# Kernel optimization log

Measured on AMD Instinct MI355X. Metric: run time of the kernel, lower is better.

The kernel has to match this reference:

```python
import jax, jax.numpy as jnp
import numpy as np

E_QUBITS = 8  # embedding dim == number of qubits


def _iqp_amplitudes(x):
    """Statevector amplitudes of qml.IQPEmbedding(x) applied to |0..0>.

    x: [..., E] real. Returns [..., 2^E] complex64.
    Circuit: H on all wires, RZ(x_i) on wire i, MultiRZ(x_i*x_j) on all pairs i<j.
    For basis state z with signs s_i = (-1)^{z_i}:
      amp(z) = 2^{-E/2} * exp(i * phi(z)),
      phi(z) = -1/2 * sum_i x_i s_i - 1/2 * sum_{i<j} x_i x_j s_i s_j
             = -L/2 - (L^2 - ||x||^2)/4,  with L = sum_i x_i s_i.
    """
    E = x.shape[-1]
    z = jnp.arange(2 ** E)
    bits = (z[:, None] >> jnp.arange(E)[None, :]) & 1          # [2^E, E]
    s = (1.0 - 2.0 * bits).astype(x.dtype)                      # (-1)^{z_i}
    L = x @ s.T                                                 # [..., 2^E]
    sq = jnp.sum(x * x, axis=-1, keepdims=True)                 # ||x||^2
    phase = -0.5 * L - 0.25 * (L * L - sq)
    return jnp.exp(1j * phase) * (2.0 ** (-E / 2.0))            # complex64


def setup_inputs() -> dict:
    key = jax.random.key(0)
    kq, kk, kv = jax.random.split(key, 3)
    B, S, E = 16, 1024, E_QUBITS
    return {
        "Q": jax.random.normal(kq, (B, S, E), dtype=jnp.float32),
        "K": jax.random.normal(kk, (B, S, E), dtype=jnp.float32),
        "V": jax.random.normal(kv, (B, S, E), dtype=jnp.float32),
    }


def reference(Q, K, V):
    # Pure-state amplitudes for every token (IQP embedding). [B,S,2^E] complex
    aq = _iqp_amplitudes(Q)
    ak = _iqp_amplitudes(K)
    # Fidelity of pure states: |<psi_q|psi_k>|^2, batched Gram matrix.
    ip = jnp.einsum("bid,bjd->bij", jnp.conj(aq), ak)          # [B,S,S] complex
    fid = jnp.real(ip * jnp.conj(ip))                           # [B,S,S] float32
    attn = 2.0 * fid - 1.0
    return jnp.einsum("bij,bje->bie", attn, V)                  # [B,S,E]
```

## Files before the change

### kernel.cpp

```cpp
#include <hip/hip_runtime.h>
#include <hip/hip_bf16.h>
#include <stdint.h>

#define NB 16
#define S_LEN 1024
#define E_Q 8

typedef float v4f __attribute__((ext_vector_type(4)));
typedef short v8s __attribute__((ext_vector_type(8)));
typedef int   v4i __attribute__((ext_vector_type(4)));

__global__ __launch_bounds__(256) void build_tables(
    const float* __restrict__ Q, const float* __restrict__ K,
    int8_t* __restrict__ Aq, int8_t* __restrict__ Kt,
    float* __restrict__ out)
{
    const int which = blockIdx.y;
    const float* X = which ? K : Q;

    if (which == 0 && blockIdx.x < 128) {
        float4 z; z.x = z.y = z.z = z.w = 0.f;
        ((float4*)out)[blockIdx.x * 256 + threadIdx.x] = z;
    }

    const int tok = blockIdx.x * 16 + (threadIdx.x >> 4);
    const int hi  = threadIdx.x & 15;
    const int zb  = hi * 16;

    const float* x = X + tok * E_Q;
    float xv[E_Q]; float sq = 0.f;
#pragma unroll
    for (int i = 0; i < E_Q; ++i) { xv[i] = x[i]; sq += xv[i] * xv[i]; }
    const float qsq = 0.25f * sq;

    float L = xv[0] + xv[1] + xv[2] + xv[3];
#pragma unroll
    for (int i = 4; i < 8; ++i) L += ((hi >> (i - 4)) & 1) ? -xv[i] : xv[i];

    __align__(16) int8_t cb[16];
    __align__(16) int8_t sb[16];

    {
        const float phi = fmaf(-0.25f, L * L, fmaf(-0.5f, L, qsq));
        float s, c; __sincosf(phi, &s, &c);
        cb[0] = (int8_t)__float2int_rn(127.f * c);
        sb[0] = (int8_t)__float2int_rn(127.f * s);
    }
#pragma unroll
    for (int n = 1; n < 16; ++n) {
        const int g  = n ^ (n >> 1);
        const int gp = (n - 1) ^ ((n - 1) >> 1);
        const int t  = __builtin_ctz(g ^ gp);
        const float twox = 2.0f * xv[t];
        L = ((g >> t) & 1) ? (L - twox) : (L + twox);
        const float phi = fmaf(-0.25f, L * L, fmaf(-0.5f, L, qsq));
        float s, c; __sincosf(phi, &s, &c);
        cb[g] = (int8_t)__float2int_rn(127.f * c);
        sb[g] = (int8_t)__float2int_rn(127.f * s);
    }

    if (which == 0) {
        int8_t* dst = Aq + (size_t)tok * 512;
        *(uint4*)(dst + zb)       = *(const uint4*)cb;
        *(uint4*)(dst + 256 + zb) = *(const uint4*)sb;
    } else {
        __align__(16) int8_t nb[16];
#pragma unroll
        for (int i = 0; i < 16; ++i) nb[i] = (int8_t)(-cb[i]);
        int8_t* dst = Kt + (size_t)tok * 768;
        *(uint4*)(dst + zb)       = *(const uint4*)cb;
        *(uint4*)(dst + 256 + zb) = *(const uint4*)sb;
        *(uint4*)(dst + 512 + zb) = *(const uint4*)nb;
    }
}

__global__ __launch_bounds__(256, 2) void qk_pv(
    const int8_t* __restrict__ Aq, const int8_t* __restrict__ Kt,
    const float* __restrict__ V, float* __restrict__ out)
{
    __shared__ __align__(16) char smem[49152];
    int8_t* lA  = (int8_t*)smem;
    int8_t* lK0 = (int8_t*)(smem + 16384);
    int8_t* lK1 = (int8_t*)(smem + 32768);
    uint16_t* lattn = (uint16_t*)smem;
    uint16_t* lVt   = (uint16_t*)(smem + 34816);

    const int jblk = blockIdx.x, iblk = blockIdx.y, b = blockIdx.z;
    const int tid  = threadIdx.x;
    const int lane = tid & 63, wv = tid >> 6;
    const int wKj = wv >> 1, wQi = wv & 1;
    const int r15 = lane & 15, qq = lane >> 4;

    const int qsw   = (tid & 7) ^ ((tid >> 3) & 7);
    const int baseA = (tid >> 3) * 512 + qsw * 16;
    const int baseK = (tid >> 3) * 768 + qsw * 16;
    const int lbase = wv * 1024;

    const int8_t* gA = Aq + (size_t)(b * S_LEN + iblk * 128) * 512;
    const int8_t* gK = Kt + (size_t)(b * S_LEN + jblk * 128) * 768;

    v4i accRe[4][4], accIm[4][4];
#pragma unroll
    for (int nj = 0; nj < 4; ++nj)
#pragma unroll
        for (int mi = 0; mi < 4; ++mi) {
            accRe[nj][mi] = (v4i)0;
            accIm[nj][mi] = (v4i)0;
        }

    for (int c = 0; c < 4; ++c) {
        __syncthreads();
        const int cbyte = c * 128;
#pragma unroll
        for (int p = 0; p < 4; ++p) {
            const int lo = p * 4096 + lbase;
            __builtin_amdgcn_global_load_lds(
                (const __attribute__((address_space(1))) void*)(gA + cbyte + baseA + p * 16384),
                (__attribute__((address_space(3))) void*)(lA + lo), 16, 0, 0);
            __builtin_amdgcn_global_load_lds(
                (const __attribute__((address_space(1))) void*)(gK + cbyte + baseK + p * 24576),
                (__attribute__((address_space(3))) void*)(lK0 + lo), 16, 0, 0);
            __builtin_amdgcn_global_load_lds(
                (const __attribute__((address_space(1))) void*)(gK + 256 + cbyte + baseK + p * 24576),
                (__attribute__((address_space(3))) void*)(lK1 + lo), 16, 0, 0);
        }
        __syncthreads();

#pragma unroll
        for (int w = 0; w < 2; ++w) {
            v4i qF[4];
#pragma unroll
            for (int mi = 0; mi < 4; ++mi) {
                const int row = wQi * 64 + mi * 16 + r15;
                qF[mi] = *(const v4i*)&lA[row * 128 + (((w << 2) | qq) ^ (row & 7)) * 16];
            }
#pragma unroll
            for (int nj = 0; nj < 4; ++nj) {
                const int rk  = wKj * 64 + nj * 16 + r15;
                const int off = rk * 128 + (((w << 2) | qq) ^ (rk & 7)) * 16;
                const v4i k0 = *(const v4i*)&lK0[off];
                const v4i k1 = *(const v4i*)&lK1[off];
#pragma unroll
                for (int mi = 0; mi < 4; ++mi) {
                    accRe[nj][mi] = __builtin_amdgcn_mfma_i32_16x16x64_i8(k0, qF[mi], accRe[nj][mi], 0, 0, 0);
                    accIm[nj][mi] = __builtin_amdgcn_mfma_i32_16x16x64_i8(k1, qF[mi], accIm[nj][mi], 0, 0, 0);
                }
            }
        }
    }

    __syncthreads();

    const float4 vreg = ((const float4*)(V + ((size_t)b * S_LEN + jblk * 128) * E_Q))[tid];

    const float sc2 = 3.0517578125e-05f / 260144641.0f;
#pragma unroll
    for (int nj = 0; nj < 4; ++nj) {
#pragma unroll
        for (int mi = 0; mi < 4; ++mi) {
            uint64_t pk = 0;
#pragma unroll
            for (int rg = 0; rg < 4; ++rg) {
                const float rf  = (float)accRe[nj][mi][rg];
                const float imf = (float)accIm[nj][mi][rg];
                const float a   = fmaf(rf * rf + imf * imf, sc2, -1.0f);
                __hip_bfloat16 ab = __float2bfloat16(a);
                pk |= (uint64_t)(*(const uint16_t*)&ab) << (16 * rg);
            }
            const int i  = wQi * 64 + mi * 16 + r15;
            const int j0 = wKj * 64 + nj * 16 + qq * 4;
            *(uint64_t*)&lattn[i * 136 + j0] = pk;
        }
    }
    {
        const int j = tid >> 1, eh = (tid & 1) * 4;
        const float vv[4] = {vreg.x, vreg.y, vreg.z, vreg.w};
#pragma unroll
        for (int c2 = 0; c2 < 4; ++c2) {
            __hip_bfloat16 vb = __float2bfloat16(vv[c2]);
            lVt[(eh + c2) * 136 + j] = *(const uint16_t*)&vb;
        }
    }
    __syncthreads();

    v8s bfr[4];
#pragma unroll
    for (int ks3 = 0; ks3 < 4; ++ks3)
        bfr[ks3] = *(const v8s*)&lVt[r15 * 136 + ks3 * 32 + qq * 8];

    float* outb = out + (((size_t)b << 10) + iblk * 128) * E_Q;
#pragma unroll
    for (int mt = 0; mt < 2; ++mt) {
        const int rowbase = (wv * 2 + mt) * 16;
        v4f accO = (v4f)0.f;
#pragma unroll
        for (int ks3 = 0; ks3 < 4; ++ks3) {
            const v8s af = *(const v8s*)&lattn[(rowbase + r15) * 136 + ks3 * 32 + qq * 8];
            accO = __builtin_amdgcn_mfma_f32_16x16x32_bf16(af, bfr[ks3], accO, 0, 0, 0);
        }
        if (r15 < E_Q) {
            const int i0 = rowbase + qq * 4;
#pragma unroll
            for (int rg = 0; rg < 4; ++rg)
                atomicAdd(&outb[(i0 + rg) * E_Q + r15], accO[rg]);
        }
    }
}

extern "C" void kernel_launch(void* const* d_in, const int* in_sizes, int n_in,
                              void* d_out, int out_size, void* d_ws, size_t ws_size,
                              hipStream_t stream) {
    const float* Q = (const float*)d_in[0];
    const float* K = (const float*)d_in[1];
    const float* V = (const float*)d_in[2];
    float* out = (float*)d_out;

    int8_t* Aq = (int8_t*)d_ws;
    int8_t* Kt = (int8_t*)((char*)d_ws + (size_t)8 * 1024 * 1024);

    build_tables<<<dim3(NB * S_LEN / 16, 2), 256, 0, stream>>>(Q, K, Aq, Kt, out);
    qk_pv<<<dim3(S_LEN / 128, S_LEN / 128, NB), 256, 0, stream>>>(Aq, Kt, V, out);
}
```

Baseline: 89.54 us.

## Double-buffer QK int8 tiles with async LDS loads and finer k-chunks

Replaces the single-buffered four-chunk load/compute loop with an eight-chunk double-buffered pipeline. Global-to-LDS loads for chunk c+2 are issued while chunk c is computed, using manual vmcnt waits and raw barriers in place of full syncthreads. The LDS layout and swizzle change to 64-byte rows, and s_setprio is raised around the MFMA block. This aims to hide global load latency behind matrix math, at the cost of more barriers and hand-tuned waitcnt logic that must stay correct.

Measured after the change: 91.59 us. +2.3%, slower.

```diff
diff --git a/kernel.cpp b/kernel.cpp
--- a/kernel.cpp
+++ b/kernel.cpp
@@ -79,9 +79,6 @@
     const float* __restrict__ V, float* __restrict__ out)
 {
     __shared__ __align__(16) char smem[49152];
-    int8_t* lA  = (int8_t*)smem;
-    int8_t* lK0 = (int8_t*)(smem + 16384);
-    int8_t* lK1 = (int8_t*)(smem + 32768);
     uint16_t* lattn = (uint16_t*)smem;
     uint16_t* lVt   = (uint16_t*)(smem + 34816);
 
@@ -91,10 +88,14 @@
     const int wKj = wv >> 1, wQi = wv & 1;
     const int r15 = lane & 15, qq = lane >> 4;
 
-    const int qsw   = (tid & 7) ^ ((tid >> 3) & 7);
-    const int baseA = (tid >> 3) * 512 + qsw * 16;
-    const int baseK = (tid >> 3) * 768 + qsw * 16;
-    const int lbase = wv * 1024;
+    const int ssw   = ((tid & 3) ^ ((tid >> 2) & 3)) << 4;
+    const int baseA = (tid >> 2) * 512 + ssw;
+    const int baseK = (tid >> 2) * 768 + ssw;
+    const int ldst  = tid * 16;
+
+    const int swz16 = (qq ^ (r15 & 3)) << 4;
+    const int offA  = wQi * 4096 + r15 * 64 + swz16;
+    const int offK  = 8192 + wKj * 4096 + r15 * 64 + swz16;
 
     const int8_t* gA = Aq + (size_t)(b * S_LEN + iblk * 128) * 512;
     const int8_t* gK = Kt + (size_t)(b * S_LEN + jblk * 128) * 768;
@@ -108,46 +109,58 @@
             accIm[nj][mi] = (v4i)0;
         }
 
-    for (int c = 0; c < 4; ++c) {
-        __syncthreads();
-        const int cbyte = c * 128;
-#pragma unroll
-        for (int p = 0; p < 4; ++p) {
-            const int lo = p * 4096 + lbase;
-            __builtin_amdgcn_global_load_lds(
-                (const __attribute__((address_space(1))) void*)(gA + cbyte + baseA + p * 16384),
-                (__attribute__((address_space(3))) void*)(lA + lo), 16, 0, 0);
-            __builtin_amdgcn_global_load_lds(
-                (const __attribute__((address_space(1))) void*)(gK + cbyte + baseK + p * 24576),
-                (__attribute__((address_space(3))) void*)(lK0 + lo), 16, 0, 0);
-            __builtin_amdgcn_global_load_lds(
-                (const __attribute__((address_space(1))) void*)(gK + 256 + cbyte + baseK + p * 24576),
-                (__attribute__((address_space(3))) void*)(lK1 + lo), 16, 0, 0);
-        }
-        __syncthreads();
-
-#pragma unroll
-        for (int w = 0; w < 2; ++w) {
+#define STAGE(cc, bb)                                                          \
+    {                                                                          \
+        const int lb0 = (bb) * 24576 + ldst;                                   \
+        _Pragma("unroll")                                                      \
+        for (int p = 0; p < 2; ++p) {                                          \
+            __builtin_amdgcn_global_load_lds(                                  \
+                (const __attribute__((address_space(1))) void*)(gA + (cc) * 64 + baseA + p * 32768), \
+                (__attribute__((address_space(3))) void*)(smem + lb0 + p * 4096), 16, 0, 0); \
+            __builtin_amdgcn_global_load_lds(                                  \
+                (const __attribute__((address_space(1))) void*)(gK + (cc) * 64 + baseK + p * 49152), \
+                (__attribute__((address_space(3))) void*)(smem + lb0 + 8192 + p * 4096), 16, 0, 0); \
+            __builtin_amdgcn_global_load_lds(                                  \
+                (const __attribute__((address_space(1))) void*)(gK + 256 + (cc) * 64 + baseK + p * 49152), \
+                (__attribute__((address_space(3))) void*)(smem + lb0 + 16384 + p * 4096), 16, 0, 0); \
+        }                                                                      \
+    }
+
+    STAGE(0, 0)
+    STAGE(1, 1)
+
+#pragma unroll
+    for (int c = 0; c < 8; ++c) {
+        if (c == 7) { asm volatile("s_waitcnt vmcnt(0)" ::: "memory"); }
+        else        { asm volatile("s_waitcnt vmcnt(6)" ::: "memory"); }
+        __builtin_amdgcn_s_barrier();
+        asm volatile("" ::: "memory");
+
+        {
+            const int8_t* lb = (const int8_t*)smem + ((c & 1) ? 24576 : 0);
             v4i qF[4];
 #pragma unroll
-            for (int mi = 0; mi < 4; ++mi) {
-                const int row = wQi * 64 + mi * 16 + r15;
-                qF[mi] = *(const v4i*)&lA[row * 128 + (((w << 2) | qq) ^ (row & 7)) * 16];
-            }
+            for (int mi = 0; mi < 4; ++mi)
+                qF[mi] = *(const v4i*)(lb + offA + mi * 1024);
+            __builtin_amdgcn_s_setprio(1);
 #pragma unroll
             for (int nj = 0; nj < 4; ++nj) {
-                const int rk  = wKj * 64 + nj * 16 + r15;
-                const int off = rk * 128 + (((w << 2) | qq) ^ (rk & 7)) * 16;
-                const v4i k0 = *(const v4i*)&lK0[off];
-                const v4i k1 = *(const v4i*)&lK1[off];
+                const v4i k0 = *(const v4i*)(lb + offK + nj * 1024);
+                const v4i k1 = *(const v4i*)(lb + offK + 8192 + nj * 1024);
 #pragma unroll
                 for (int mi = 0; mi < 4; ++mi) {
                     accRe[nj][mi] = __builtin_amdgcn_mfma_i32_16x16x64_i8(k0, qF[mi], accRe[nj][mi], 0, 0, 0);
                     accIm[nj][mi] = __builtin_amdgcn_mfma_i32_16x16x64_i8(k1, qF[mi], accIm[nj][mi], 0, 0, 0);
                 }
             }
-        }
-    }
+            __builtin_amdgcn_s_setprio(0);
+        }
+
+        asm volatile("" ::: "memory");
+        __builtin_amdgcn_s_barrier();
+        if (c < 6) STAGE(c + 2, c & 1)
+    }
+#undef STAGE
 
     __syncthreads();
 
```
